# Kernel tuning notes

Hardware: AMD Instinct MI355X
Metric: run time of the kernel (lower is better)

Reference implementation:

```python
import jax, jax.numpy as jnp
import numpy as np

B, T, FB, C = 2, 256, 128, 128
H_T, H_F, BAND = 4, 4, 16
INNER = 4 * C


def setup_inputs() -> dict:
    key = jax.random.key(0)
    ks = jax.random.split(key, 8)
    g = lambda k, shp: jax.random.normal(k, shp, jnp.float32) * 0.02
    return {
        "x": jax.random.normal(ks[0], (B, T, FB, C), jnp.float32),
        # temporal pre-norm + MHA (in_proj [3C,C], out_proj [C,C])
        "ln_t_w": jnp.ones((C,), jnp.float32), "ln_t_b": jnp.zeros((C,), jnp.float32),
        "t_wi": g(ks[1], (3 * C, C)), "t_bi": jnp.zeros((3 * C,), jnp.float32),
        "t_wo": g(ks[2], (C, C)), "t_bo": jnp.zeros((C,), jnp.float32),
        # frequency pre-norm + MHA
        "ln_f_w": jnp.ones((C,), jnp.float32), "ln_f_b": jnp.zeros((C,), jnp.float32),
        "f_wi": g(ks[3], (3 * C, C)), "f_bi": jnp.zeros((3 * C,), jnp.float32),
        "f_wo": g(ks[4], (C, C)), "f_bo": jnp.zeros((C,), jnp.float32),
        # FFN pre-norm + two linears
        "ln_n_w": jnp.ones((C,), jnp.float32), "ln_n_b": jnp.zeros((C,), jnp.float32),
        "w1": g(ks[5], (INNER, C)), "b1": jnp.zeros((INNER,), jnp.float32),
        "w2": g(ks[6], (C, INNER)), "b2": jnp.zeros((C,), jnp.float32),
    }


def _ln(x, w, b, eps=1e-5):
    mu = x.mean(-1, keepdims=True)
    var = ((x - mu) ** 2).mean(-1, keepdims=True)
    return (x - mu) * jax.lax.rsqrt(var + eps) * w + b


def _mha(x, wi, bi, wo, bo, h, mask):
    """torch.nn.MultiheadAttention equivalent. x: [..., S, C], mask: additive [S, S]."""
    c = x.shape[-1]
    dh = c // h
    qkv = x @ wi.T + bi
    q, k, v = jnp.split(qkv, 3, axis=-1)
    split = lambda t: t.reshape(t.shape[:-1] + (h, dh)).swapaxes(-2, -3)  # [..., h, S, dh]
    q, k, v = split(q), split(k), split(v)
    scores = jnp.einsum('...hqd,...hkd->...hqk', q, k) * (1.0 / np.sqrt(dh)) + mask
    attn = jax.nn.softmax(scores, axis=-1)
    o = jnp.einsum('...hqk,...hkd->...hqd', attn, v)
    o = o.swapaxes(-2, -3).reshape(x.shape)
    return o @ wo.T + bo


def _causal_mask(n):
    i = jnp.arange(n)
    return jnp.where(i[:, None] >= i[None, :], 0.0, -jnp.inf).astype(jnp.float32)


def _band_mask(n, band):
    i = jnp.arange(n)
    return jnp.where(jnp.abs(i[:, None] - i[None, :]) <= band, 0.0, -jnp.inf).astype(jnp.float32)


def reference(x, ln_t_w, ln_t_b, t_wi, t_bi, t_wo, t_bo,
              ln_f_w, ln_f_b, f_wi, f_bi, f_wo, f_bo,
              ln_n_w, ln_n_b, w1, b1, w2, b2):
    cm = _causal_mask(x.shape[1])      # [T, T]
    bm = _band_mask(x.shape[2], BAND)  # [F, F]
    # temporal causal MHSA per frequency bin (pre-norm residual)
    xt = _ln(x, ln_t_w, ln_t_b).transpose(0, 2, 1, 3)  # [B, F, T, C]
    x = x + _mha(xt, t_wi, t_bi, t_wo, t_bo, H_T, cm).transpose(0, 2, 1, 3)
    # banded local MHSA over frequency per time step
    xf = _ln(x, ln_f_w, ln_f_b)  # [B, T, F, C]
    x = x + _mha(xf, f_wi, f_bi, f_wo, f_bo, H_F, bm)
    # FFN (Linear -> exact GELU -> Linear)
    xn = _ln(x, ln_n_w, ln_n_b)
    h = jax.nn.gelu(xn @ w1.T + b1, approximate=False)
    x = x + (h @ w2.T + b2)
    return x
```

## Files before the change

kernel.cpp:

```cpp
#include <hip/hip_runtime.h>
#include <math.h>

typedef __bf16 bf16;
typedef __bf16 bf16x8 __attribute__((ext_vector_type(8)));
typedef __bf16 bf16x4 __attribute__((ext_vector_type(4)));
typedef __bf16 bf16x2 __attribute__((ext_vector_type(2)));
typedef float f32x4 __attribute__((ext_vector_type(4)));
typedef float f32x2 __attribute__((ext_vector_type(2)));
typedef float f32x16 __attribute__((ext_vector_type(16)));
typedef unsigned int u32;
typedef unsigned int u32x4 __attribute__((ext_vector_type(4)));

#define AS1 __attribute__((address_space(1)))
#define AS3 __attribute__((address_space(3)))

static __device__ __forceinline__ f32x4 mfma16(bf16x8 a, bf16x8 b, f32x4 c) {
    return __builtin_amdgcn_mfma_f32_16x16x32_bf16(a, b, c, 0, 0, 0);
}
static __device__ __forceinline__ f32x16 mfma32(bf16x8 a, bf16x8 b, f32x16 c) {
    return __builtin_amdgcn_mfma_f32_32x32x16_bf16(a, b, c, 0, 0, 0);
}
static __device__ __forceinline__ u32 pk2(float a, float b) {
    bf16x2 v; v[0] = (bf16)a; v[1] = (bf16)b;
    return __builtin_bit_cast(u32, v);
}
static __device__ __forceinline__ float gelu_f(float x) {
    float u = 0.7978845608f * x * __builtin_fmaf(0.044715f, x * x, 1.0f);
    float e = __expf(2.0f * u);
    return x - x * __builtin_amdgcn_rcpf(e + 1.0f);
}

__global__ __launch_bounds__(256) void cvt_w6(
    const float* __restrict__ s0, const float* __restrict__ s1,
    const float* __restrict__ s2, const float* __restrict__ s3,
    const float* __restrict__ s4, const float* __restrict__ s5,
    bf16* __restrict__ dst)
{
    int i = (blockIdx.x * 256 + threadIdx.x) * 4;
    const float* src; int off;
    if      (i <  49152) { src = s0; off = 0; }
    else if (i <  65536) { src = s1; off = 49152; }
    else if (i < 114688) { src = s2; off = 65536; }
    else if (i < 131072) { src = s3; off = 114688; }
    else if (i < 196608) { src = s4; off = 131072; }
    else                 { src = s5; off = 196608; }
    f32x4 v = *(const f32x4*)&src[i - off];
    bf16x4 b;
    b[0] = (bf16)v[0]; b[1] = (bf16)v[1]; b[2] = (bf16)v[2]; b[3] = (bf16)v[3];
    *(bf16x4*)&dst[i] = b;
}

template<int OUT_BF16, int RES, int RESBF, int GELU_, int LNA, int RMAP, int KT, int NT>
__global__ __launch_bounds__(256) void gemm_rw(
    const bf16* __restrict__ A, const bf16* __restrict__ W,
    const float* __restrict__ bias, const void* __restrict__ res,
    void* __restrict__ outp,
    const float* __restrict__ xf, const float* __restrict__ lnaw,
    const float* __restrict__ lnab)
{
    constexpr int N = NT * 128;
    __shared__ __align__(16) bf16 Bs[128 * 64];
    const int tid  = threadIdx.x;
    const int lane = tid & 63;
    const int w    = tid >> 6;
    const int li = lane & 15, g = lane >> 4;
    const int m0 = blockIdx.x * 64;
    const int arow = m0 + w * 16 + li;
    int srow = arow;
    if constexpr (RMAP) {
        int b = arow >> 15, t = (arow >> 7) & 255, f = arow & 127;
        srow = (b << 15) + (f << 8) + t;
    }
    const bf16* ap = A + (size_t)srow * KT;

    bf16x8 afrag[4];
    if constexpr (LNA) {
        int b = arow >> 15, f = (arow >> 8) & 127, t = arow & 255;
        const float* xp = xf + (((size_t)b * 256 + t) * 128 + f) * 128;
        f32x4 cv[8];
        #pragma unroll
        for (int cc = 0; cc < 4; ++cc) {
            cv[2 * cc]     = *(const f32x4*)&xp[cc * 32 + g * 8];
            cv[2 * cc + 1] = *(const f32x4*)&xp[cc * 32 + g * 8 + 4];
        }
        float sm = 0.f, sq = 0.f;
        #pragma unroll
        for (int i = 0; i < 8; ++i)
            #pragma unroll
            for (int j = 0; j < 4; ++j) { float v = cv[i][j]; sm += v; sq += v * v; }
        sm += __shfl_xor(sm, 16); sm += __shfl_xor(sm, 32);
        sq += __shfl_xor(sq, 16); sq += __shfl_xor(sq, 32);
        float mu = sm * 0.0078125f;
        float rs = rsqrtf(sq * 0.0078125f - mu * mu + 1e-5f);
        #pragma unroll
        for (int cc = 0; cc < 4; ++cc) {
            f32x4 w0 = *(const f32x4*)&lnaw[cc * 32 + g * 8];
            f32x4 w1 = *(const f32x4*)&lnaw[cc * 32 + g * 8 + 4];
            f32x4 b0 = *(const f32x4*)&lnab[cc * 32 + g * 8];
            f32x4 b1 = *(const f32x4*)&lnab[cc * 32 + g * 8 + 4];
            #pragma unroll
            for (int j = 0; j < 4; ++j) {
                afrag[cc][j]     = (bf16)((cv[2 * cc][j]     - mu) * rs * w0[j] + b0[j]);
                afrag[cc][4 + j] = (bf16)((cv[2 * cc + 1][j] - mu) * rs * w1[j] + b1[j]);
            }
        }
    } else if constexpr (KT == 128) {
        #pragma unroll
        for (int cc = 0; cc < 4; ++cc)
            afrag[cc] = *(const bf16x8*)&ap[cc * 32 + g * 8];
    }

    #pragma unroll
    for (int t = 0; t < NT; ++t) {
        const int n0 = t * 128;
        f32x4 acc[8] = {};

        #pragma unroll
        for (int k0 = 0; k0 < KT; k0 += 64) {
            #pragma unroll
            for (int it = 0; it < 4; ++it) {
                int idx = it * 256 + tid;
                int brow = idx >> 3, bch = idx & 7;
                const bf16* gp = W + (size_t)(n0 + brow) * KT + k0 + ((bch ^ (brow & 7)) * 8);
                __builtin_amdgcn_global_load_lds((AS1 void*)gp, (AS3 void*)(Bs + idx * 8), 16, 0, 0);
            }
            bf16x8 av0, av1;
            if constexpr (KT != 128) {
                av0 = *(const bf16x8*)&ap[k0 + g * 8];
                av1 = *(const bf16x8*)&ap[k0 + 32 + g * 8];
            }
            __syncthreads();
            #pragma unroll
            for (int kk = 0; kk < 2; ++kk) {
                bf16x8 av;
                if constexpr (KT == 128) av = afrag[(k0 >> 5) + kk];
                else                     av = kk ? av1 : av0;
                #pragma unroll
                for (int j = 0; j < 8; ++j) {
                    int brow = j * 16 + li;
                    int bch = (kk * 4 + g) ^ (li & 7);
                    bf16x8 bv = *(const bf16x8*)&Bs[brow * 64 + bch * 8];
                    acc[j] = mfma16(av, bv, acc[j]);
                }
            }
            __syncthreads();
        }

        float bcol[8];
        #pragma unroll
        for (int j = 0; j < 8; ++j) bcol[j] = bias[n0 + j * 16 + li];

        const int row0 = m0 + w * 16 + g * 4;
        #pragma unroll
        for (int r = 0; r < 4; ++r) {
            int row = row0 + r;
            #pragma unroll
            for (int j = 0; j < 8; ++j) {
                size_t off = (size_t)row * N + n0 + j * 16 + li;
                float v = acc[j][r] + bcol[j];
                if constexpr (RES) {
                    if constexpr (RESBF) v += (float)((const bf16*)res)[off];
                    else                 v += ((const float*)res)[off];
                }
                if constexpr (GELU_) v = gelu_f(v);
                if constexpr (OUT_BF16) ((bf16*)outp)[off] = (bf16)v;
                else                    ((float*)outp)[off] = v;
            }
        }
    }
}

template<int MODE, int RESBF>
__global__ __launch_bounds__(256) void attn_fused(
    const bf16* __restrict__ qkv, const bf16* __restrict__ Wo,
    const float* __restrict__ bo, const void* __restrict__ res,
    bf16* __restrict__ xc, bf16* __restrict__ xn,
    const float* __restrict__ lnw, const float* __restrict__ lnb)
{
    constexpr int S = (MODE == 0) ? 256 : 128;
    __shared__ __align__(16) bf16 o_lds[32 * 136];
    __shared__ float red[32][4][2];
    const int lane = threadIdx.x & 63;
    const int w = threadIdx.x >> 6;
    const int hi = lane >> 5;
    const int q31 = lane & 31;
    const int s = blockIdx.x;
    const int qb = blockIdx.y * 32;
    const int q = qb + q31;

    const size_t base = (size_t)s * S * 384;
    const bf16* qp = qkv + base + w * 32;
    const bf16* kp = qp + 128;
    const bf16* vp = qp + 256 + q31;

    const float sc = 0.17677669529663687f;
    bf16x8 qr0 = *(const bf16x8*)&qp[(size_t)q * 384 + hi * 8];
    bf16x8 qr1 = *(const bf16x8*)&qp[(size_t)q * 384 + 16 + hi * 8];
    bf16x8 qf0, qf1;
    #pragma unroll
    for (int e = 0; e < 8; ++e) {
        qf0[e] = (bf16)((float)qr0[e] * sc);
        qf1[e] = (bf16)((float)qr1[e] * sc);
    }

    f32x16 O = {};
    float m = -1e30f, l = 0.f;

    int klo, khi;
    if constexpr (MODE == 0) { klo = 0; khi = qb + 32; }
    else {
        klo = (qb > 16 ? (qb - 16) : 0) & ~31;
        khi = (qb + 48 < S) ? (qb + 48) : S;
    }

    for (int k0 = klo; k0 < khi; k0 += 32) {
        bf16x8 kf0 = *(const bf16x8*)&kp[(size_t)(k0 + q31) * 384 + hi * 8];
        bf16x8 kf1 = *(const bf16x8*)&kp[(size_t)(k0 + q31) * 384 + 16 + hi * 8];
        bf16x8 vf1, vf2;
        #pragma unroll
        for (int e = 0; e < 8; ++e) {
            vf1[e] = vp[(size_t)(k0 + hi * 8 + e) * 384];
            vf2[e] = vp[(size_t)(k0 + 16 + hi * 8 + e) * 384];
        }

        f32x16 st = {};
        st = mfma32(kf0, qf0, st);
        st = mfma32(kf1, qf1, st);

        if (MODE == 1 || k0 + 32 > qb) {
            #pragma unroll
            for (int r = 0; r < 16; ++r) {
                int krow = k0 + (r & 3) + 8 * (r >> 2) + 4 * hi;
                bool ok;
                if constexpr (MODE == 0) ok = (krow <= q);
                else { int d = krow - q; ok = (d <= 16 && d >= -16); }
                st[r] = ok ? st[r] : -3.0e38f;
            }
        }
        float mx = st[0];
        #pragma unroll
        for (int r = 1; r < 16; ++r) mx = fmaxf(mx, st[r]);
        mx = fmaxf(mx, __shfl_xor(mx, 32));
        float mn = fmaxf(m, mx);
        float resc = __expf(m - mn);
        m = mn;
        float ps = 0.f;
        #pragma unroll
        for (int r = 0; r < 16; ++r) {
            float p = __expf(st[r] - mn);
            st[r] = p;
            ps += p;
        }
        ps += __shfl_xor(ps, 32);
        l = l * resc + ps;
        #pragma unroll
        for (int r = 0; r < 16; ++r) O[r] *= resc;

        u32 c01 = pk2(st[0], st[1]),   c23 = pk2(st[2], st[3]);
        u32 c45 = pk2(st[4], st[5]),   c67 = pk2(st[6], st[7]);
        u32 c89 = pk2(st[8], st[9]),   cAB = pk2(st[10], st[11]);
        u32 cCD = pk2(st[12], st[13]), cEF = pk2(st[14], st[15]);
        u32 x01 = __shfl_xor((int)c01, 32), x23 = __shfl_xor((int)c23, 32);
        u32 x45 = __shfl_xor((int)c45, 32), x67 = __shfl_xor((int)c67, 32);
        u32 x89 = __shfl_xor((int)c89, 32), xAB = __shfl_xor((int)cAB, 32);
        u32 xCD = __shfl_xor((int)cCD, 32), xEF = __shfl_xor((int)cEF, 32);
        u32x4 b1w = hi ? u32x4{x45, x67, c45, c67} : u32x4{c01, c23, x01, x23};
        u32x4 b2w = hi ? u32x4{xCD, xEF, cCD, cEF} : u32x4{c89, cAB, x89, xAB};
        bf16x8 B1 = __builtin_bit_cast(bf16x8, b1w);
        bf16x8 B2 = __builtin_bit_cast(bf16x8, b2w);

        O = mfma32(vf1, B1, O);
        O = mfma32(vf2, B2, O);
    }

    float inv = 1.f / l;
    #pragma unroll
    for (int mb = 0; mb < 4; ++mb) {
        bf16x4 ov;
        #pragma unroll
        for (int j = 0; j < 4; ++j) ov[j] = (bf16)(O[mb * 4 + j] * inv);
        *(bf16x4*)&o_lds[q31 * 136 + w * 32 + mb * 8 + hi * 4] = ov;
    }
    __syncthreads();

    const int li = lane & 15, g = lane >> 4;
    bf16x8 af[2][4];
    #pragma unroll
    for (int mi = 0; mi < 2; ++mi)
        #pragma unroll
        for (int kk = 0; kk < 4; ++kk)
            af[mi][kk] = *(const bf16x8*)&o_lds[(mi * 16 + li) * 136 + kk * 32 + g * 8];

    f32x4 acc[2][2] = {};
    #pragma unroll
    for (int ni = 0; ni < 2; ++ni) {
        #pragma unroll
        for (int kk = 0; kk < 4; ++kk) {
            bf16x8 bv = *(const bf16x8*)&Wo[(size_t)(w * 32 + ni * 16 + li) * 128 + kk * 32 + g * 8];
            acc[0][ni] = mfma16(af[0][kk], bv, acc[0][ni]);
            acc[1][ni] = mfma16(af[1][kk], bv, acc[1][ni]);
        }
    }

    float vals[2][2][4];
    #pragma unroll
    for (int mi = 0; mi < 2; ++mi) {
        #pragma unroll
        for (int r = 0; r < 4; ++r) {
            int lr = qb + mi * 16 + g * 4 + r;
            size_t rrow;
            if constexpr (MODE == 0) {
                int b = s >> 7, f = s & 127;
                rrow = ((size_t)(b * 256 + lr)) * 128 + f;
            } else {
                int b = s >> 8, t = s & 255;
                rrow = (size_t)b * 32768 + (size_t)lr * 256 + t;
            }
            #pragma unroll
            for (int ni = 0; ni < 2; ++ni) {
                int col = w * 32 + ni * 16 + li;
                float v = acc[mi][ni][r] + bo[col];
                if constexpr (RESBF) v += (float)((const bf16*)res)[rrow * 128 + col];
                else                 v += ((const float*)res)[rrow * 128 + col];
                vals[mi][ni][r] = v;
            }
        }
    }
    #pragma unroll
    for (int mi = 0; mi < 2; ++mi) {
        #pragma unroll
        for (int r = 0; r < 4; ++r) {
            float sm = vals[mi][0][r] + vals[mi][1][r];
            float sq = vals[mi][0][r] * vals[mi][0][r] + vals[mi][1][r] * vals[mi][1][r];
            #pragma unroll
            for (int off = 1; off < 16; off <<= 1) {
                sm += __shfl_xor(sm, off);
                sq += __shfl_xor(sq, off);
            }
            if (li == 0) {
                red[mi * 16 + g * 4 + r][w][0] = sm;
                red[mi * 16 + g * 4 + r][w][1] = sq;
            }
        }
    }
    __syncthreads();
    #pragma unroll
    for (int mi = 0; mi < 2; ++mi) {
        #pragma unroll
        for (int r = 0; r < 4; ++r) {
            int mrow = mi * 16 + g * 4 + r;
            f32x4 p0 = *(const f32x4*)&red[mrow][0][0];
            f32x4 p1 = *(const f32x4*)&red[mrow][2][0];
            float smt = p0[0] + p0[2] + p1[0] + p1[2];
            float sqt = p0[1] + p0[3] + p1[1] + p1[3];
            float mu = smt * 0.0078125f;
            float rs = rsqrtf(sqt * 0.0078125f - mu * mu + 1e-5f);
            size_t woff = ((size_t)s * S + qb + mrow) * 128;
            #pragma unroll
            for (int ni = 0; ni < 2; ++ni) {
                int col = w * 32 + ni * 16 + li;
                float v = vals[mi][ni][r];
                xc[woff + col] = (bf16)v;
                xn[woff + col] = (bf16)((v - mu) * rs * lnw[col] + lnb[col]);
            }
        }
    }
}

extern "C" void kernel_launch(void* const* d_in, const int* in_sizes, int n_in,
                              void* d_out, int out_size, void* d_ws, size_t ws_size,
                              hipStream_t stream) {
    const float* x      = (const float*)d_in[0];
    const float* ln_t_w = (const float*)d_in[1];
    const float* ln_t_b = (const float*)d_in[2];
    const float* t_wi   = (const float*)d_in[3];
    const float* t_bi   = (const float*)d_in[4];
    const float* t_wo   = (const float*)d_in[5];
    const float* t_bo   = (const float*)d_in[6];
    const float* ln_f_w = (const float*)d_in[7];
    const float* ln_f_b = (const float*)d_in[8];
    const float* f_wi   = (const float*)d_in[9];
    const float* f_bi   = (const float*)d_in[10];
    const float* f_wo   = (const float*)d_in[11];
    const float* f_bo   = (const float*)d_in[12];
    const float* ln_n_w = (const float*)d_in[13];
    const float* ln_n_b = (const float*)d_in[14];
    const float* w1     = (const float*)d_in[15];
    const float* b1     = (const float*)d_in[16];
    const float* w2     = (const float*)d_in[17];
    const float* b2     = (const float*)d_in[18];

    char* ws = (char*)d_ws;
    bf16* wbf  = (bf16*)ws;
    bf16* xn   = (bf16*)(ws + 524288);
    bf16* qkvh = (bf16*)(ws + 524288 + 16777216);
    bf16* xcA  = (bf16*)(ws + 524288 + 16777216 + 67108864 + 16777216);
    bf16* xcB  = (bf16*)(ws + 524288 + 16777216 + 67108864 + 2 * 16777216);
    float* out = (float*)d_out;

    const bf16* twi_b = wbf + 0;
    const bf16* two_b = wbf + 49152;
    const bf16* fwi_b = wbf + 65536;
    const bf16* fwo_b = wbf + 114688;
    const bf16* w1_b  = wbf + 131072;
    const bf16* w2_b  = wbf + 196608;

    cvt_w6<<<256, 256, 0, stream>>>(t_wi, t_wo, f_wi, f_wo, w1, w2, wbf);

    gemm_rw<1, 0, 0, 0, 1, 0, 128, 3><<<1024, 256, 0, stream>>>(
        nullptr, twi_b, t_bi, nullptr, qkvh, x, ln_t_w, ln_t_b);
    attn_fused<0, 0><<<dim3(256, 8), 256, 0, stream>>>(
        qkvh, two_b, t_bo, x, xcA, xn, ln_f_w, ln_f_b);

    gemm_rw<1, 0, 0, 0, 0, 1, 128, 3><<<1024, 256, 0, stream>>>(
        xn, fwi_b, f_bi, nullptr, qkvh, nullptr, nullptr, nullptr);
    attn_fused<1, 1><<<dim3(512, 4), 256, 0, stream>>>(
        qkvh, fwo_b, f_bo, xcA, xcB, xn, ln_n_w, ln_n_b);

    gemm_rw<1, 0, 0, 1, 0, 0, 128, 4><<<1024, 256, 0, stream>>>(
        xn, w1_b, b1, nullptr, qkvh, nullptr, nullptr, nullptr);
    gemm_rw<0, 1, 1, 0, 0, 0, 512, 1><<<1024, 256, 0, stream>>>(
        qkvh, w2_b, b2, xcB, out, nullptr, nullptr, nullptr);

    (void)in_sizes; (void)n_in; (void)out_size; (void)ws_size;
}
```

Baseline: 166.8 us.

## Process two 32-row query tiles per attention block to reuse K/V loads

Each attention block now handles 64 query rows as two 32-row sub-tiles that share every K/V fragment load, halving the grid size in the query dimension. Per-sub-tile activity and diagonal-mask flags skip out-of-range key tiles for causal and banded modes. The output projection and LayerNorm epilogue are widened to 64 rows. This cuts redundant global K/V reads and Wo loads, but raises register pressure and halves the number of blocks, which could lower occupancy and parallelism.

```diff
diff --git a/kernel.cpp b/kernel.cpp
--- a/kernel.cpp
+++ b/kernel.cpp
@@ -178,15 +178,14 @@
     const float* __restrict__ lnw, const float* __restrict__ lnb)
 {
     constexpr int S = (MODE == 0) ? 256 : 128;
-    __shared__ __align__(16) bf16 o_lds[32 * 136];
-    __shared__ float red[32][4][2];
+    __shared__ __align__(16) bf16 o_lds[64 * 136];
+    __shared__ float red[64][4][2];
     const int lane = threadIdx.x & 63;
     const int w = threadIdx.x >> 6;
     const int hi = lane >> 5;
     const int q31 = lane & 31;
     const int s = blockIdx.x;
-    const int qb = blockIdx.y * 32;
-    const int q = qb + q31;
+    const int qb = blockIdx.y * 64;
 
     const size_t base = (size_t)s * S * 384;
     const bf16* qp = qkv + base + w * 32;
@@ -194,23 +193,29 @@
     const bf16* vp = qp + 256 + q31;
 
     const float sc = 0.17677669529663687f;
-    bf16x8 qr0 = *(const bf16x8*)&qp[(size_t)q * 384 + hi * 8];
-    bf16x8 qr1 = *(const bf16x8*)&qp[(size_t)q * 384 + 16 + hi * 8];
-    bf16x8 qf0, qf1;
-    #pragma unroll
-    for (int e = 0; e < 8; ++e) {
-        qf0[e] = (bf16)((float)qr0[e] * sc);
-        qf1[e] = (bf16)((float)qr1[e] * sc);
-    }
-
-    f32x16 O = {};
-    float m = -1e30f, l = 0.f;
+    bf16x8 qA0, qA1, qB0, qB1;
+    {
+        bf16x8 r0 = *(const bf16x8*)&qp[(size_t)(qb + q31) * 384 + hi * 8];
+        bf16x8 r1 = *(const bf16x8*)&qp[(size_t)(qb + q31) * 384 + 16 + hi * 8];
+        bf16x8 r2 = *(const bf16x8*)&qp[(size_t)(qb + 32 + q31) * 384 + hi * 8];
+        bf16x8 r3 = *(const bf16x8*)&qp[(size_t)(qb + 32 + q31) * 384 + 16 + hi * 8];
+        #pragma unroll
+        for (int e = 0; e < 8; ++e) {
+            qA0[e] = (bf16)((float)r0[e] * sc);
+            qA1[e] = (bf16)((float)r1[e] * sc);
+            qB0[e] = (bf16)((float)r2[e] * sc);
+            qB1[e] = (bf16)((float)r3[e] * sc);
+        }
+    }
+
+    f32x16 OA = {}, OB = {};
+    float mA = -1e30f, lA = 0.f, mB = -1e30f, lB = 0.f;
 
     int klo, khi;
-    if constexpr (MODE == 0) { klo = 0; khi = qb + 32; }
+    if constexpr (MODE == 0) { klo = 0; khi = qb + 64; }
     else {
         klo = (qb > 16 ? (qb - 16) : 0) & ~31;
-        khi = (qb + 48 < S) ? (qb + 48) : S;
+        khi = (qb + 80 < S) ? (qb + 80) : S;
     }
 
     for (int k0 = klo; k0 < khi; k0 += 32) {
@@ -223,98 +228,116 @@
             vf2[e] = vp[(size_t)(k0 + 16 + hi * 8 + e) * 384];
         }
 
-        f32x16 st = {};
-        st = mfma32(kf0, qf0, st);
-        st = mfma32(kf1, qf1, st);
-
-        if (MODE == 1 || k0 + 32 > qb) {
+        auto set_step = [&](f32x16& O, float& m, float& l,
+                            bf16x8 q0, bf16x8 q1, int qrow, bool doMask) {
+            f32x16 st = {};
+            st = mfma32(kf0, q0, st);
+            st = mfma32(kf1, q1, st);
+            if (doMask) {
+                #pragma unroll
+                for (int r = 0; r < 16; ++r) {
+                    int krow = k0 + (r & 3) + 8 * (r >> 2) + 4 * hi;
+                    bool ok;
+                    if constexpr (MODE == 0) ok = (krow <= qrow);
+                    else { int d = krow - qrow; ok = (d <= 16 && d >= -16); }
+                    st[r] = ok ? st[r] : -3.0e38f;
+                }
+            }
+            float mx = st[0];
+            #pragma unroll
+            for (int r = 1; r < 16; ++r) mx = fmaxf(mx, st[r]);
+            mx = fmaxf(mx, __shfl_xor(mx, 32));
+            float mn = fmaxf(m, mx);
+            float resc = __expf(m - mn);
+            m = mn;
+            float ps = 0.f;
             #pragma unroll
             for (int r = 0; r < 16; ++r) {
-                int krow = k0 + (r & 3) + 8 * (r >> 2) + 4 * hi;
-                bool ok;
-                if constexpr (MODE == 0) ok = (krow <= q);
-                else { int d = krow - q; ok = (d <= 16 && d >= -16); }
-                st[r] = ok ? st[r] : -3.0e38f;
-            }
-        }
-        float mx = st[0];
-        #pragma unroll
-        for (int r = 1; r < 16; ++r) mx = fmaxf(mx, st[r]);
-        mx = fmaxf(mx, __shfl_xor(mx, 32));
-        float mn = fmaxf(m, mx);
-        float resc = __expf(m - mn);
-        m = mn;
-        float ps = 0.f;
-        #pragma unroll
-        for (int r = 0; r < 16; ++r) {
-            float p = __expf(st[r] - mn);
-            st[r] = p;
-            ps += p;
-        }
-        ps += __shfl_xor(ps, 32);
-        l = l * resc + ps;
-        #pragma unroll
-        for (int r = 0; r < 16; ++r) O[r] *= resc;
-
-        u32 c01 = pk2(st[0], st[1]),   c23 = pk2(st[2], st[3]);
-        u32 c45 = pk2(st[4], st[5]),   c67 = pk2(st[6], st[7]);
-        u32 c89 = pk2(st[8], st[9]),   cAB = pk2(st[10], st[11]);
-        u32 cCD = pk2(st[12], st[13]), cEF = pk2(st[14], st[15]);
-        u32 x01 = __shfl_xor((int)c01, 32), x23 = __shfl_xor((int)c23, 32);
-        u32 x45 = __shfl_xor((int)c45, 32), x67 = __shfl_xor((int)c67, 32);
-        u32 x89 = __shfl_xor((int)c89, 32), xAB = __shfl_xor((int)cAB, 32);
-        u32 xCD = __shfl_xor((int)cCD, 32), xEF = __shfl_xor((int)cEF, 32);
-        u32x4 b1w = hi ? u32x4{x45, x67, c45, c67} : u32x4{c01, c23, x01, x23};
-        u32x4 b2w = hi ? u32x4{xCD, xEF, cCD, cEF} : u32x4{c89, cAB, x89, xAB};
-        bf16x8 B1 = __builtin_bit_cast(bf16x8, b1w);
-        bf16x8 B2 = __builtin_bit_cast(bf16x8, b2w);
-
-        O = mfma32(vf1, B1, O);
-        O = mfma32(vf2, B2, O);
-    }
-
-    float inv = 1.f / l;
+                float p = __expf(st[r] - mn);
+                st[r] = p;
+                ps += p;
+            }
+            ps += __shfl_xor(ps, 32);
+            l = l * resc + ps;
+            #pragma unroll
+            for (int r = 0; r < 16; ++r) O[r] *= resc;
+
+            u32 c01 = pk2(st[0], st[1]),   c23 = pk2(st[2], st[3]);
+            u32 c45 = pk2(st[4], st[5]),   c67 = pk2(st[6], st[7]);
+            u32 c89 = pk2(st[8], st[9]),   cAB = pk2(st[10], st[11]);
+            u32 cCD = pk2(st[12], st[13]), cEF = pk2(st[14], st[15]);
+            u32 x01 = __shfl_xor((int)c01, 32), x23 = __shfl_xor((int)c23, 32);
+            u32 x45 = __shfl_xor((int)c45, 32), x67 = __shfl_xor((int)c67, 32);
+            u32 x89 = __shfl_xor((int)c89, 32), xAB = __shfl_xor((int)cAB, 32);
+            u32 xCD = __shfl_xor((int)cCD, 32), xEF = __shfl_xor((int)cEF, 32);
+            u32x4 b1w = hi ? u32x4{x45, x67, c45, c67} : u32x4{c01, c23, x01, x23};
+            u32x4 b2w = hi ? u32x4{xCD, xEF, cCD, cEF} : u32x4{c89, cAB, x89, xAB};
+            bf16x8 B1 = __builtin_bit_cast(bf16x8, b1w);
+            bf16x8 B2 = __builtin_bit_cast(bf16x8, b2w);
+
+            O = mfma32(vf1, B1, O);
+            O = mfma32(vf2, B2, O);
+        };
+
+        bool actA, actB, dgA, dgB;
+        if constexpr (MODE == 0) {
+            actA = (k0 <= qb); actB = true;
+            dgA = (k0 == qb);  dgB = (k0 == qb + 32);
+        } else {
+            actA = (k0 <= qb + 47); actB = (k0 + 15 >= qb);
+            dgA = true; dgB = true;
+        }
+        if (actA) set_step(OA, mA, lA, qA0, qA1, qb + q31, dgA);
+        if (actB) set_step(OB, mB, lB, qB0, qB1, qb + 32 + q31, dgB);
+    }
+
+    float invA = 1.f / lA, invB = 1.f / lB;
     #pragma unroll
     for (int mb = 0; mb < 4; ++mb) {
-        bf16x4 ov;
-        #pragma unroll
-        for (int j = 0; j < 4; ++j) ov[j] = (bf16)(O[mb * 4 + j] * inv);
-        *(bf16x4*)&o_lds[q31 * 136 + w * 32 + mb * 8 + hi * 4] = ov;
+        bf16x4 ovA, ovB;
+        #pragma unroll
+        for (int j = 0; j < 4; ++j) {
+            ovA[j] = (bf16)(OA[mb * 4 + j] * invA);
+            ovB[j] = (bf16)(OB[mb * 4 + j] * invB);
+        }
+        *(bf16x4*)&o_lds[q31 * 136 + w * 32 + mb * 8 + hi * 4] = ovA;
+        *(bf16x4*)&o_lds[(32 + q31) * 136 + w * 32 + mb * 8 + hi * 4] = ovB;
     }
     __syncthreads();
 
     const int li = lane & 15, g = lane >> 4;
-    bf16x8 af[2][4];
-    #pragma unroll
-    for (int mi = 0; mi < 2; ++mi)
+    bf16x8 af[4][4];
+    #pragma unroll
+    for (int mi = 0; mi < 4; ++mi)
         #pragma unroll
         for (int kk = 0; kk < 4; ++kk)
             af[mi][kk] = *(const bf16x8*)&o_lds[(mi * 16 + li) * 136 + kk * 32 + g * 8];
 
-    f32x4 acc[2][2] = {};
+    f32x4 acc[4][2] = {};
     #pragma unroll
     for (int ni = 0; ni < 2; ++ni) {
         #pragma unroll
         for (int kk = 0; kk < 4; ++kk) {
             bf16x8 bv = *(const bf16x8*)&Wo[(size_t)(w * 32 + ni * 16 + li) * 128 + kk * 32 + g * 8];
-            acc[0][ni] = mfma16(af[0][kk], bv, acc[0][ni]);
-            acc[1][ni] = mfma16(af[1][kk], bv, acc[1][ni]);
-        }
-    }
-
-    float vals[2][2][4];
-    #pragma unroll
-    for (int mi = 0; mi < 2; ++mi) {
+            #pragma unroll
+            for (int mi = 0; mi < 4; ++mi)
+                acc[mi][ni] = mfma16(af[mi][kk], bv, acc[mi][ni]);
+        }
+    }
+
+    float vals[4][2][4];
+    #pragma unroll
+    for (int mi = 0; mi < 4; ++mi) {
         #pragma unroll
         for (int r = 0; r < 4; ++r) {
-            int lr = qb + mi * 16 + g * 4 + r;
+            int lrl = mi * 16 + g * 4 + r;
             size_t rrow;
             if constexpr (MODE == 0) {
                 int b = s >> 7, f = s & 127;
-                rrow = ((size_t)(b * 256 + lr)) * 128 + f;
+                rrow = ((size_t)(b * 256 + qb + lrl)) * 128 + f;
             } else {
                 int b = s >> 8, t = s & 255;
-                rrow = (size_t)b * 32768 + (size_t)lr * 256 + t;
+                rrow = (size_t)b * 32768 + (size_t)(qb + lrl) * 256 + t;
             }
             #pragma unroll
             for (int ni = 0; ni < 2; ++ni) {
@@ -327,7 +350,7 @@
         }
     }
     #pragma unroll
-    for (int mi = 0; mi < 2; ++mi) {
+    for (int mi = 0; mi < 4; ++mi) {
         #pragma unroll
         for (int r = 0; r < 4; ++r) {
             float sm = vals[mi][0][r] + vals[mi][1][r];
@@ -345,7 +368,7 @@
     }
     __syncthreads();
     #pragma unroll
-    for (int mi = 0; mi < 2; ++mi) {
+    for (int mi = 0; mi < 4; ++mi) {
         #pragma unroll
         for (int r = 0; r < 4; ++r) {
             int mrow = mi * 16 + g * 4 + r;
@@ -409,12 +432,12 @@
 
     gemm_rw<1, 0, 0, 0, 1, 0, 128, 3><<<1024, 256, 0, stream>>>(
         nullptr, twi_b, t_bi, nullptr, qkvh, x, ln_t_w, ln_t_b);
-    attn_fused<0, 0><<<dim3(256, 8), 256, 0, stream>>>(
+    attn_fused<0, 0><<<dim3(256, 4), 256, 0, stream>>>(
         qkvh, two_b, t_bo, x, xcA, xn, ln_f_w, ln_f_b);
 
     gemm_rw<1, 0, 0, 0, 0, 1, 128, 3><<<1024, 256, 0, stream>>>(
         xn, fwi_b, f_bi, nullptr, qkvh, nullptr, nullptr, nullptr);
-    attn_fused<1, 1><<<dim3(512, 4), 256, 0, stream>>>(
+    attn_fused<1, 1><<<dim3(512, 2), 256, 0, stream>>>(
         qkvh, fwo_b, f_bo, xcA, xcB, xn, ln_n_w, ln_n_b);
 
     gemm_rw<1, 0, 0, 1, 0, 0, 128, 4><<<1024, 256, 0, stream>>>(
```

Result: no change. 167.1 us (+0.2%).
